# Kernel tuning notes

Measured on AMD Instinct MI355X. Metric: run time of the kernel, lower is better.

The kernel has to match this reference:

```python
import jax, jax.numpy as jnp
import numpy as np

B, M, H, D = 2, 16384, 8, 64
HID = H * D
SEG = 128          # segment_lengths[0]
DIL = 2            # dilation_rates[0]


def _hilbert_perm(m):
    """perm[d] = row-major token index of the d-th point on the Hilbert curve
    over an n x n grid (n = sqrt(m), power of 2). Vectorized d2xy."""
    n = int(round(np.sqrt(m)))
    assert n * n == m and (n & (n - 1)) == 0
    t = np.arange(m, dtype=np.int64)
    x = np.zeros(m, np.int64)
    y = np.zeros(m, np.int64)
    s = 1
    while s < n:
        rx = 1 & (t // 2)
        ry = 1 & (t ^ rx)
        swap = ry == 0
        flip = swap & (rx == 1)
        xf = np.where(flip, s - 1 - x, x)
        yf = np.where(flip, s - 1 - y, y)
        x, y = np.where(swap, yf, xf), np.where(swap, xf, yf)
        x = x + s * rx
        y = y + s * ry
        t = t // 4
        s *= 2
    return y * n + x


_PERM = _hilbert_perm(M)
_INV = np.empty(M, np.int64)
_INV[_PERM] = np.arange(M)
PERM = jnp.asarray(_PERM)
INV_PERM = jnp.asarray(_INV)


def setup_inputs() -> dict:
    key = jax.random.key(0)
    ks = jax.random.split(key, 8)
    sc = 0.02
    return {
        "q": jax.random.normal(ks[0], (B, M, H, D), jnp.float32),
        "k": jax.random.normal(ks[1], (B, M, H, D), jnp.float32),
        "v": jax.random.normal(ks[2], (B, M, H, D), jnp.float32),
        # wrapper projections (nn.Linear without bias; stored [in, out])
        "Wq": jax.random.normal(ks[3], (HID, HID), jnp.float32) * sc,
        "Wk": jax.random.normal(ks[4], (HID, HID), jnp.float32) * sc,
        "Wv": jax.random.normal(ks[5], (HID, HID), jnp.float32) * sc,
        # HilbertAttentionCore fused qkv projection
        "Wqkv": jax.random.normal(ks[6], (HID, 3 * HID), jnp.float32) * sc,
        # wrapper output projection
        "Wout": jax.random.normal(ks[7], (HID, HID), jnp.float32) * sc,
    }


def _hilbert_attention(x, Wqkv):
    """x: [B, M, HID] -> [B, M, HID]. Hilbert reorder + segmented dilated attn."""
    b, m, _ = x.shape
    qkv = x @ Wqkv                                    # [B, M, 3*HID]
    qkv = qkv.reshape(b, m, 3, H, D)
    # Hilbert-curve reordering of the sequence (gather)
    qkv = qkv[:, PERM]                                # [B, M, 3, H, D]
    nseg = m // SEG
    g = SEG // DIL                                    # tokens per dilated group
    # [B, nseg, g, DIL, 3, H, D]: group r holds positions r, r+DIL, ... in seg
    qkv = qkv.reshape(b, nseg, g, DIL, 3, H, D)
    qh, kh, vh = qkv[..., 0, :, :], qkv[..., 1, :, :], qkv[..., 2, :, :]
    scale = 1.0 / jnp.sqrt(jnp.asarray(D, x.dtype))
    # attention within each (segment, dilation-group): t,s index the g tokens
    scores = jnp.einsum("bntrhd,bnsrhd->bnrhts", qh, kh) * scale
    attn = jax.nn.softmax(scores, axis=-1)
    out = jnp.einsum("bnrhts,bnsrhd->bntrhd", attn, vh)
    out = out.reshape(b, m, H, D)
    # inverse Hilbert reordering (scatter back)
    out = out[:, INV_PERM]
    return out.reshape(b, m, HID)


def reference(q, k, v, Wq, Wk, Wv, Wqkv, Wout):
    b, m, h, d = q.shape
    q_flat = q.reshape(b, m, h * d)
    k_flat = k.reshape(b, m, h * d)
    v_flat = v.reshape(b, m, h * d)
    x = (q_flat @ Wq + k_flat @ Wk + v_flat @ Wv) / 3.0
    out = _hilbert_attention(x, Wqkv)
    out = out @ Wout
    return out.reshape(b, m, h, d)
```

## Files before the change

kernel.cpp:

```cpp
#include <hip/hip_runtime.h>
#include <hip/hip_bf16.h>
#include <stdint.h>


typedef __bf16 bf16_t;
typedef __bf16 bf16x8 __attribute__((ext_vector_type(8)));
typedef float  f32x4  __attribute__((ext_vector_type(4)));

#define DEVI __device__ __forceinline__
#define BAR __builtin_amdgcn_s_barrier()

static constexpr int Mtok = 16384;
static constexpr int ROWS = 32768;

DEVI void gload_lds16(const void* g, void* l) {
  __builtin_amdgcn_global_load_lds(
      (__attribute__((address_space(1))) uint32_t*)(uintptr_t)g,
      (__attribute__((address_space(3))) uint32_t*)(uint32_t)(uintptr_t)l,
      16, 0, 0);
}

__global__ void k_perm(int* __restrict__ perm) {
  int d = blockIdx.x * 256 + threadIdx.x;
  if (d >= Mtok) return;
  int t = d, x = 0, y = 0;
  for (int s = 1; s < 128; s <<= 1) {
    int rx = (t >> 1) & 1;
    int ry = (t ^ rx) & 1;
    if (ry == 0) {
      if (rx == 1) { x = s - 1 - x; y = s - 1 - y; }
      int tmp = x; x = y; y = tmp;
    }
    x += s * rx;
    y += s * ry;
    t >>= 2;
  }
  perm[d] = y * 128 + x;
}

__global__ void k_prep_w(const float* __restrict__ Wq, const float* __restrict__ Wk,
                         const float* __restrict__ Wv, const float* __restrict__ Wqkv,
                         const float* __restrict__ Wout,
                         bf16_t* __restrict__ W1t, bf16_t* __restrict__ Wqkvt,
                         bf16_t* __restrict__ Woutt) {
  const int tid = blockIdx.x * 256 + threadIdx.x;
  const int stride = gridDim.x * 256;
  for (int i = tid; i < 512 * 1536; i += stride) {
    int n = i / 1536, kk = i % 1536;
    const float* W = (kk < 512) ? Wq : (kk < 1024 ? Wk : Wv);
    W1t[i] = (bf16_t)(W[(kk & 511) * 512 + n] * (1.0f / 3.0f));
  }
  for (int i = tid; i < 1536 * 512; i += stride) {
    int n = i / 512, kk = i % 512;
    Wqkvt[i] = (bf16_t)Wqkv[kk * 1536 + n];
  }
  for (int i = tid; i < 512 * 512; i += stride) {
    int n = i / 512, kk = i % 512;
    Woutt[i] = (bf16_t)Wout[kk * 512 + n];
  }
}

DEVI void stageB(const bf16_t* Bb, int Kdim, int k0, bf16_t* dst, int qsel,
                 int tid, int cswz) {
  int r = tid >> 3;
  int rb0 = (r >> 5) * 64 + qsel * 32 + (r & 31);
  const bf16_t* g = Bb + (long)rb0 * Kdim + k0 + cswz * 8;
  gload_lds16(g, dst + rb0 * 64 + (tid & 7) * 8);
  gload_lds16(g + (long)128 * Kdim, dst + (rb0 + 128) * 64 + (tid & 7) * 8);
}

DEVI void stageA(const bf16_t* Ab, int Kdim, int k0, bf16_t* dst, int qsel,
                 int tid, int cswz) {
  int r = tid >> 3;
  int row0 = r + qsel * 64;
  const bf16_t* g = Ab + (long)row0 * Kdim + k0 + cswz * 8;
  gload_lds16(g, dst + row0 * 64 + (tid & 7) * 8);
  gload_lds16(g + (long)128 * Kdim, dst + (row0 + 128) * 64 + (tid & 7) * 8);
}

#define LOAD_AF(AF, QM, BUF)                                                   \
  _Pragma("unroll") for (int m = 0; m < 4; m++) {                              \
    int row = wm * 128 + (QM) * 64 + m * 16 + l15;                             \
    AF[m][0] = *(const bf16x8*)((BUF) + row * 64 + cb0 * 8);                   \
    AF[m][1] = *(const bf16x8*)((BUF) + row * 64 + cb1 * 8);                   \
  }
#define LOAD_BG(BG, QN, BUF)                                                   \
  _Pragma("unroll") for (int n = 0; n < 2; n++) {                              \
    int row = wn * 64 + (QN) * 32 + n * 16 + l15;                              \
    BG[n][0] = *(const bf16x8*)((BUF) + row * 64 + cb0 * 8);                   \
    BG[n][1] = *(const bf16x8*)((BUF) + row * 64 + cb1 * 8);                   \
  }
#define QUAD(QM, QN, AF, BG)                                                   \
  do {                                                                         \
    __builtin_amdgcn_s_setprio(1);                                             \
    _Pragma("unroll") for (int kh = 0; kh < 2; kh++)                           \
    _Pragma("unroll") for (int m = 0; m < 4; m++)                              \
    _Pragma("unroll") for (int n = 0; n < 2; n++)                              \
      acc[(QM)*4+m][(QN)*2+n] = __builtin_amdgcn_mfma_f32_16x16x32_bf16(       \
          AF[m][kh], BG[n][kh], acc[(QM)*4+m][(QN)*2+n], 0, 0, 0);             \
    __builtin_amdgcn_s_setprio(0);                                             \
  } while (0)

template <bool OUTF32>
__global__ __launch_bounds__(512, 2) void k_gemm256(const bf16_t* __restrict__ A,
                                                    const bf16_t* __restrict__ Bt,
                                                    bf16_t* __restrict__ Cb,
                                                    float* __restrict__ Cf,
                                                    int Ndim, int Kdim) {
  __shared__ bf16_t lds[4 * 16384];
  const int tid = threadIdx.x;
  const int lane = tid & 63, w = tid >> 6;
  const int wm = w >> 2, wn = w & 3;
  const int l15 = lane & 15, l4 = lane >> 4;
  const int cb0 = l4 ^ (l15 & 7), cb1 = cb0 ^ 4;
  const int cswz = (tid & 7) ^ ((tid >> 3) & 7);
  const long arow0 = (long)blockIdx.y * 256;
  const long bcol0 = (long)blockIdx.x * 256;
  const bf16_t* Ab = A + arow0 * Kdim;
  const bf16_t* Bb = Bt + bcol0 * Kdim;
  const int NT = Kdim >> 6;

  bf16_t* Acur = lds;
  bf16_t* Bcur = lds + 16384;
  bf16_t* Anxt = lds + 32768;
  bf16_t* Bnxt = lds + 49152;

  f32x4 acc[8][4] = {};

  stageA(Ab, Kdim, 0, Acur, 0, tid, cswz);
  stageA(Ab, Kdim, 0, Acur, 1, tid, cswz);
  stageB(Bb, Kdim, 0, Bcur, 0, tid, cswz);
  stageB(Bb, Kdim, 0, Bcur, 1, tid, cswz);
  stageA(Ab, Kdim, 64, Anxt, 0, tid, cswz);
  stageB(Bb, Kdim, 64, Bnxt, 1, tid, cswz);
  asm volatile("s_waitcnt vmcnt(4)" ::: "memory");
  BAR;

  for (int t = 0; t < NT; t++) {
    bf16x8 af[4][2], bg0[2][2], bg1[2][2];
    LOAD_AF(af, 0, Acur);
    LOAD_BG(bg0, 0, Bcur);
    if (t + 1 < NT) stageB(Bb, Kdim, (t + 1) * 64, Bnxt, 0, tid, cswz);
    BAR;
    QUAD(0, 0, af, bg0);
    BAR;
    LOAD_BG(bg1, 1, Bcur);
    if (t + 1 < NT) stageA(Ab, Kdim, (t + 1) * 64, Anxt, 1, tid, cswz);
    BAR;
    QUAD(0, 1, af, bg1);
    BAR;
    LOAD_AF(af, 1, Acur);
    if (t + 2 < NT) stageA(Ab, Kdim, (t + 2) * 64, Acur, 0, tid, cswz);
    BAR;
    QUAD(1, 1, af, bg1);
    BAR;
    LOAD_BG(bg0, 0, Bcur);
    if (t + 2 < NT) stageB(Bb, Kdim, (t + 2) * 64, Bcur, 1, tid, cswz);
    BAR;
    QUAD(1, 0, af, bg0);
    if (t + 2 < NT) { asm volatile("s_waitcnt vmcnt(4)" ::: "memory"); }
    else            { asm volatile("s_waitcnt vmcnt(0)" ::: "memory"); }
    BAR;
    bf16_t* tA = Acur; Acur = Anxt; Anxt = tA;
    bf16_t* tB = Bcur; Bcur = Bnxt; Bnxt = tB;
  }

#pragma unroll
  for (int i = 0; i < 8; i++) {
#pragma unroll
    for (int j = 0; j < 4; j++) {
      long row = arow0 + wm * 128 + i * 16 + l4 * 4;
      long col = bcol0 + wn * 64 + j * 16 + l15;
#pragma unroll
      for (int r = 0; r < 4; r++) {
        if constexpr (OUTF32) Cf[(row + r) * Ndim + col] = acc[i][j][r];
        else                  Cb[(row + r) * Ndim + col] = (bf16_t)acc[i][j][r];
      }
    }
  }
}

DEVI const float* selsrc(int tt, const float* q, const float* k, const float* v) {
  return tt < 8 ? q : (tt < 16 ? k : v);
}

DEVI void loadAh(const float* S, long grow, int colf, float4* pa) {
  const float* p0 = S + grow * 512 + colf;
  pa[0] = *(const float4*)(p0);
  pa[1] = *(const float4*)(p0 + 4);
  const float* p1 = p0 + 128 * 512;
  pa[2] = *(const float4*)(p1);
  pa[3] = *(const float4*)(p1 + 4);
}

DEVI void writeAh(bf16_t* dst, int rbase, int cbt, const float4* pa) {
  bf16x8 o0, o1;
  o0[0] = (bf16_t)pa[0].x; o0[1] = (bf16_t)pa[0].y; o0[2] = (bf16_t)pa[0].z; o0[3] = (bf16_t)pa[0].w;
  o0[4] = (bf16_t)pa[1].x; o0[5] = (bf16_t)pa[1].y; o0[6] = (bf16_t)pa[1].z; o0[7] = (bf16_t)pa[1].w;
  o1[0] = (bf16_t)pa[2].x; o1[1] = (bf16_t)pa[2].y; o1[2] = (bf16_t)pa[2].z; o1[3] = (bf16_t)pa[2].w;
  o1[4] = (bf16_t)pa[3].x; o1[5] = (bf16_t)pa[3].y; o1[6] = (bf16_t)pa[3].z; o1[7] = (bf16_t)pa[3].w;
  int sw = (cbt ^ (rbase & 7)) * 8;
  *(bf16x8*)(dst + rbase * 64 + sw) = o0;
  *(bf16x8*)(dst + (rbase + 128) * 64 + sw) = o1;
}

__global__ __launch_bounds__(512, 2) void k_gemm1f(const float* __restrict__ q,
                                                   const float* __restrict__ k,
                                                   const float* __restrict__ v,
                                                   const bf16_t* __restrict__ Bt,
                                                   bf16_t* __restrict__ Cb,
                                                   int Ndim) {
  constexpr int Kdim = 1536;
  constexpr int NT = 24;
  __shared__ bf16_t lds[4 * 16384];
  const int tid = threadIdx.x;
  const int lane = tid & 63, w = tid >> 6;
  const int wm = w >> 2, wn = w & 3;
  const int l15 = lane & 15, l4 = lane >> 4;
  const int cb0 = l4 ^ (l15 & 7), cb1 = cb0 ^ 4;
  const int cswz = (tid & 7) ^ ((tid >> 3) & 7);
  const int cbt = tid & 7, rA = tid >> 3;
  const long arow0 = (long)blockIdx.y * 256;
  const long bcol0 = (long)blockIdx.x * 256;
  const bf16_t* Bb = Bt + bcol0 * Kdim;

  bf16_t* Acur = lds;
  bf16_t* Bcur = lds + 16384;
  bf16_t* Anxt = lds + 32768;
  bf16_t* Bnxt = lds + 49152;

  f32x4 acc[8][4] = {};
  float4 pa0[4], pa1[4];

  loadAh(selsrc(0, q, k, v), arow0 + rA,      (cbt << 3), pa0);
  loadAh(selsrc(0, q, k, v), arow0 + rA + 64, (cbt << 3), pa1);
  writeAh(Acur, rA,      cbt, pa0);
  writeAh(Acur, rA + 64, cbt, pa1);
  stageB(Bb, Kdim, 0, Bcur, 0, tid, cswz);
  stageB(Bb, Kdim, 0, Bcur, 1, tid, cswz);
  loadAh(selsrc(1, q, k, v), arow0 + rA, 64 + (cbt << 3), pa0);
  writeAh(Anxt, rA, cbt, pa0);
  stageB(Bb, Kdim, 64, Bnxt, 1, tid, cswz);
  loadAh(selsrc(1, q, k, v), arow0 + rA + 64,  64 + (cbt << 3), pa1);
  loadAh(selsrc(2, q, k, v), arow0 + rA,      128 + (cbt << 3), pa0);
  asm volatile("s_waitcnt vmcnt(18)" ::: "memory");
  asm volatile("s_waitcnt lgkmcnt(0)" ::: "memory");
  BAR;

  for (int t = 0; t < NT; t++) {
    bf16x8 af[4][2], bg0[2][2], bg1[2][2];
    LOAD_AF(af, 0, Acur);
    LOAD_BG(bg0, 0, Bcur);
    if (t + 1 < NT) stageB(Bb, Kdim, (t + 1) * 64, Bnxt, 0, tid, cswz);
    BAR;
    QUAD(0, 0, af, bg0);
    BAR;
    LOAD_BG(bg1, 1, Bcur);
    if (t + 1 < NT) writeAh(Anxt, rA + 64, cbt, pa1);
    if (t + 2 < NT) loadAh(selsrc(t + 2, q, k, v), arow0 + rA + 64,
                           (((t + 2) & 7) << 6) + (cbt << 3), pa1);
    BAR;
    QUAD(0, 1, af, bg1);
    BAR;
    LOAD_AF(af, 1, Acur);
    if (t + 2 < NT) writeAh(Acur, rA, cbt, pa0);
    if (t + 3 < NT) loadAh(selsrc(t + 3, q, k, v), arow0 + rA,
                           (((t + 3) & 7) << 6) + (cbt << 3), pa0);
    BAR;
    QUAD(1, 1, af, bg1);
    BAR;
    LOAD_BG(bg0, 0, Bcur);
    if (t + 2 < NT) stageB(Bb, Kdim, (t + 2) * 64, Bcur, 1, tid, cswz);
    BAR;
    QUAD(1, 0, af, bg0);
    if (t + 3 < NT)      { asm volatile("s_waitcnt vmcnt(18)" ::: "memory"); }
    else if (t + 2 < NT) { asm volatile("s_waitcnt vmcnt(10)" ::: "memory"); }
    else                 { asm volatile("s_waitcnt vmcnt(0)"  ::: "memory"); }
    asm volatile("s_waitcnt lgkmcnt(0)" ::: "memory");
    BAR;
    bf16_t* tA = Acur; Acur = Anxt; Anxt = tA;
    bf16_t* tB = Bcur; Bcur = Bnxt; Bnxt = tB;
  }

#pragma unroll
  for (int i = 0; i < 8; i++) {
#pragma unroll
    for (int j = 0; j < 4; j++) {
      long row = arow0 + wm * 128 + i * 16 + l4 * 4;
      long col = bcol0 + wn * 64 + j * 16 + l15;
#pragma unroll
      for (int r = 0; r < 4; r++)
        Cb[(row + r) * Ndim + col] = (bf16_t)acc[i][j][r];
    }
  }
}

__global__ __launch_bounds__(256, 2) void k_attn(const bf16_t* __restrict__ QKV,
                                                 const int* __restrict__ perm,
                                                 bf16_t* __restrict__ ATT) {
  __shared__ bf16_t Vt[2][64 * 64];
  __shared__ bf16_t P[2][64 * 64];
  __shared__ bf16_t O[128 * 64];
  __shared__ int perml[128];
  const int n = blockIdx.x, h = blockIdx.y, b = blockIdx.z;
  const int t = threadIdx.x;
  const int lane = t & 63, w = t >> 6;
  const int l15 = lane & 15, l4 = lane >> 4;

  if (t < 128) perml[t] = perm[n * 128 + t];
  __syncthreads();

#pragma unroll
  for (int it = 0; it < 4; it++) {
    int c = t + it * 256;
    int tok = c >> 3, c8 = c & 7;
    long j = (long)b * Mtok + perml[tok];
    bf16x8 vv = *(const bf16x8*)(QKV + j * 1536 + 1024 + h * 64 + c8 * 8);
    int grp = tok & 1, s = tok >> 1;
    bf16_t* vt = Vt[grp];
#pragma unroll
    for (int i = 0; i < 8; i++) {
      int d = c8 * 8 + i;
      vt[d * 64 + (s ^ ((d & 7) << 3))] = vv[i];
    }
  }

  const int grp = w >> 1, th = w & 1;

  f32x4 sc[2][4] = {};
#pragma unroll
  for (int ks = 0; ks < 2; ks++) {
    bf16x8 aq[2], bk[4];
#pragma unroll
    for (int tf = 0; tf < 2; tf++) {
      int tq = th * 32 + tf * 16 + l15;
      long j = (long)b * Mtok + perml[tq * 2 + grp];
      aq[tf] = *(const bf16x8*)(QKV + j * 1536 + h * 64 + ks * 32 + l4 * 8);
    }
#pragma unroll
    for (int sf = 0; sf < 4; sf++) {
      int s = sf * 16 + l15;
      long j = (long)b * Mtok + perml[s * 2 + grp];
      bk[sf] = *(const bf16x8*)(QKV + j * 1536 + 512 + h * 64 + ks * 32 + l4 * 8);
    }
#pragma unroll
    for (int tf = 0; tf < 2; tf++)
#pragma unroll
      for (int sf = 0; sf < 4; sf++)
        sc[tf][sf] = __builtin_amdgcn_mfma_f32_16x16x32_bf16(aq[tf], bk[sf], sc[tf][sf], 0, 0, 0);
  }

  const float scale = 0.125f;
#pragma unroll
  for (int tf = 0; tf < 2; tf++) {
#pragma unroll
    for (int r = 0; r < 4; r++) {
      float mx = fmaxf(fmaxf(sc[tf][0][r], sc[tf][1][r]), fmaxf(sc[tf][2][r], sc[tf][3][r]));
      mx = fmaxf(mx, __shfl_xor(mx, 1, 64));
      mx = fmaxf(mx, __shfl_xor(mx, 2, 64));
      mx = fmaxf(mx, __shfl_xor(mx, 4, 64));
      mx = fmaxf(mx, __shfl_xor(mx, 8, 64));
      float p0 = __expf((sc[tf][0][r] - mx) * scale);
      float p1 = __expf((sc[tf][1][r] - mx) * scale);
      float p2 = __expf((sc[tf][2][r] - mx) * scale);
      float p3 = __expf((sc[tf][3][r] - mx) * scale);
      float sum = p0 + p1 + p2 + p3;
      sum += __shfl_xor(sum, 1, 64);
      sum += __shfl_xor(sum, 2, 64);
      sum += __shfl_xor(sum, 4, 64);
      sum += __shfl_xor(sum, 8, 64);
      float inv = 1.0f / sum;
      int trow = th * 32 + tf * 16 + l4 * 4 + r;
      int sw = (trow & 7) << 3;
      bf16_t* pp = P[grp];
      pp[trow * 64 + ((l15     ) ^ sw)] = (bf16_t)(p0 * inv);
      pp[trow * 64 + ((l15 + 16) ^ sw)] = (bf16_t)(p1 * inv);
      pp[trow * 64 + ((l15 + 32) ^ sw)] = (bf16_t)(p2 * inv);
      pp[trow * 64 + ((l15 + 48) ^ sw)] = (bf16_t)(p3 * inv);
    }
  }
  __syncthreads();

  f32x4 oacc[2][4] = {};
#pragma unroll
  for (int ks = 0; ks < 2; ks++) {
    bf16x8 ap[2], bv[4];
#pragma unroll
    for (int tf = 0; tf < 2; tf++) {
      int trow = th * 32 + tf * 16 + l15;
      int cb = (ks * 4 + l4) ^ (trow & 7);
      ap[tf] = *(const bf16x8*)(P[grp] + trow * 64 + cb * 8);
    }
#pragma unroll
    for (int df = 0; df < 4; df++) {
      int d = df * 16 + l15;
      int cb = (ks * 4 + l4) ^ (d & 7);
      bv[df] = *(const bf16x8*)(Vt[grp] + d * 64 + cb * 8);
    }
#pragma unroll
    for (int tf = 0; tf < 2; tf++)
#pragma unroll
      for (int df = 0; df < 4; df++)
        oacc[tf][df] = __builtin_amdgcn_mfma_f32_16x16x32_bf16(ap[tf], bv[df], oacc[tf][df], 0, 0, 0);
  }

#pragma unroll
  for (int tf = 0; tf < 2; tf++)
#pragma unroll
    for (int df = 0; df < 4; df++)
#pragma unroll
      for (int r = 0; r < 4; r++) {
        int trow = th * 32 + tf * 16 + l4 * 4 + r;
        int tok = trow * 2 + grp;
        O[tok * 64 + df * 16 + l15] = (bf16_t)oacc[tf][df][r];
      }
  __syncthreads();
#pragma unroll
  for (int it = 0; it < 4; it++) {
    int c = t + it * 256;
    int tok = c >> 3, c8 = c & 7;
    long j = (long)b * Mtok + perml[tok];
    *(bf16x8*)(ATT + j * 512 + h * 64 + c8 * 8) = *(const bf16x8*)(O + tok * 64 + c8 * 8);
  }
}

extern "C" void kernel_launch(void* const* d_in, const int* in_sizes, int n_in,
                              void* d_out, int out_size, void* d_ws, size_t ws_size,
                              hipStream_t stream) {
  const float* q    = (const float*)d_in[0];
  const float* k    = (const float*)d_in[1];
  const float* v    = (const float*)d_in[2];
  const float* Wq   = (const float*)d_in[3];
  const float* Wk   = (const float*)d_in[4];
  const float* Wv   = (const float*)d_in[5];
  const float* Wqkv = (const float*)d_in[6];
  const float* Wout = (const float*)d_in[7];

  char* ws = (char*)d_ws;
  const size_t QKV_BYTES = (size_t)ROWS * 1536 * 2;
  const size_t X_BYTES   = (size_t)ROWS * 512 * 2;
  bf16_t* QKV   = (bf16_t*)ws;
  bf16_t* X     = (bf16_t*)(ws + QKV_BYTES);
  bf16_t* W1t   = (bf16_t*)(ws + QKV_BYTES + X_BYTES);
  bf16_t* Wqkvt = W1t + 512 * 1536;
  bf16_t* Woutt = Wqkvt + 1536 * 512;
  int*    perm  = (int*)(Woutt + 512 * 512);

  k_perm<<<64, 256, 0, stream>>>(perm);
  k_prep_w<<<512, 256, 0, stream>>>(Wq, Wk, Wv, Wqkv, Wout, W1t, Wqkvt, Woutt);
  k_gemm1f<<<dim3(2, 128), 512, 0, stream>>>(q, k, v, W1t, X, 512);
  k_gemm256<false><<<dim3(6, 128), 512, 0, stream>>>(X, Wqkvt, QKV, nullptr, 1536, 512);
  k_attn<<<dim3(128, 8, 2), 256, 0, stream>>>(QKV, perm, X);
  k_gemm256<true><<<dim3(2, 128), 512, 0, stream>>>(X, Woutt, nullptr, (float*)d_out, 512, 512);
}
```

Baseline: 233.5 us.

## Fuse QKV projection, segmented attention and output projection into one kernel

Replaces the QKV GEMM, the attention kernel and the output-projection GEMM with a single kernel per (segment, dilation group, batch). Each block gathers its 64 permuted X rows into LDS, computes per-head Q/K/V with double-buffered weight tiles, runs attention in LDS and accumulates the output projection in registers. Results are scattered straight to the fp32 output. This removes the large bf16 QKV and attention intermediates in global memory and two kernel launches. In exchange, every block re-streams the full reordered Wqkv and Wout weights, heavy LDS use limits occupancy to one block per CU, and only half the waves do the attention step.

```diff
diff --git a/kernel.cpp b/kernel.cpp
--- a/kernel.cpp
+++ b/kernel.cpp
@@ -5,6 +5,7 @@
 
 typedef __bf16 bf16_t;
 typedef __bf16 bf16x8 __attribute__((ext_vector_type(8)));
+typedef __bf16 bf16x4 __attribute__((ext_vector_type(4)));
 typedef float  f32x4  __attribute__((ext_vector_type(4)));
 
 #define DEVI __device__ __forceinline__
@@ -41,7 +42,7 @@
 __global__ void k_prep_w(const float* __restrict__ Wq, const float* __restrict__ Wk,
                          const float* __restrict__ Wv, const float* __restrict__ Wqkv,
                          const float* __restrict__ Wout,
-                         bf16_t* __restrict__ W1t, bf16_t* __restrict__ Wqkvt,
+                         bf16_t* __restrict__ W1t, bf16_t* __restrict__ Wqkvr,
                          bf16_t* __restrict__ Woutt) {
   const int tid = blockIdx.x * 256 + threadIdx.x;
   const int stride = gridDim.x * 256;
@@ -50,9 +51,12 @@
     const float* W = (kk < 512) ? Wq : (kk < 1024 ? Wk : Wv);
     W1t[i] = (bf16_t)(W[(kk & 511) * 512 + n] * (1.0f / 3.0f));
   }
-  for (int i = tid; i < 1536 * 512; i += stride) {
-    int n = i / 512, kk = i % 512;
-    Wqkvt[i] = (bf16_t)Wqkv[kk * 1536 + n];
+  for (int i = tid; i < 8 * 192 * 512; i += stride) {
+    int h = i / (192 * 512);
+    int rem = i % (192 * 512);
+    int row = rem / 512, kk = rem % 512;
+    int gsel = row >> 6, c = row & 63;
+    Wqkvr[i] = (bf16_t)Wqkv[kk * 1536 + gsel * 512 + h * 64 + c];
   }
   for (int i = tid; i < 512 * 512; i += stride) {
     int n = i / 512, kk = i % 512;
@@ -67,15 +71,6 @@
   const bf16_t* g = Bb + (long)rb0 * Kdim + k0 + cswz * 8;
   gload_lds16(g, dst + rb0 * 64 + (tid & 7) * 8);
   gload_lds16(g + (long)128 * Kdim, dst + (rb0 + 128) * 64 + (tid & 7) * 8);
-}
-
-DEVI void stageA(const bf16_t* Ab, int Kdim, int k0, bf16_t* dst, int qsel,
-                 int tid, int cswz) {
-  int r = tid >> 3;
-  int row0 = r + qsel * 64;
-  const bf16_t* g = Ab + (long)row0 * Kdim + k0 + cswz * 8;
-  gload_lds16(g, dst + row0 * 64 + (tid & 7) * 8);
-  gload_lds16(g + (long)128 * Kdim, dst + (row0 + 128) * 64 + (tid & 7) * 8);
 }
 
 #define LOAD_AF(AF, QM, BUF)                                                   \
@@ -100,85 +95,6 @@
           AF[m][kh], BG[n][kh], acc[(QM)*4+m][(QN)*2+n], 0, 0, 0);             \
     __builtin_amdgcn_s_setprio(0);                                             \
   } while (0)
-
-template <bool OUTF32>
-__global__ __launch_bounds__(512, 2) void k_gemm256(const bf16_t* __restrict__ A,
-                                                    const bf16_t* __restrict__ Bt,
-                                                    bf16_t* __restrict__ Cb,
-                                                    float* __restrict__ Cf,
-                                                    int Ndim, int Kdim) {
-  __shared__ bf16_t lds[4 * 16384];
-  const int tid = threadIdx.x;
-  const int lane = tid & 63, w = tid >> 6;
-  const int wm = w >> 2, wn = w & 3;
-  const int l15 = lane & 15, l4 = lane >> 4;
-  const int cb0 = l4 ^ (l15 & 7), cb1 = cb0 ^ 4;
-  const int cswz = (tid & 7) ^ ((tid >> 3) & 7);
-  const long arow0 = (long)blockIdx.y * 256;
-  const long bcol0 = (long)blockIdx.x * 256;
-  const bf16_t* Ab = A + arow0 * Kdim;
-  const bf16_t* Bb = Bt + bcol0 * Kdim;
-  const int NT = Kdim >> 6;
-
-  bf16_t* Acur = lds;
-  bf16_t* Bcur = lds + 16384;
-  bf16_t* Anxt = lds + 32768;
-  bf16_t* Bnxt = lds + 49152;
-
-  f32x4 acc[8][4] = {};
-
-  stageA(Ab, Kdim, 0, Acur, 0, tid, cswz);
-  stageA(Ab, Kdim, 0, Acur, 1, tid, cswz);
-  stageB(Bb, Kdim, 0, Bcur, 0, tid, cswz);
-  stageB(Bb, Kdim, 0, Bcur, 1, tid, cswz);
-  stageA(Ab, Kdim, 64, Anxt, 0, tid, cswz);
-  stageB(Bb, Kdim, 64, Bnxt, 1, tid, cswz);
-  asm volatile("s_waitcnt vmcnt(4)" ::: "memory");
-  BAR;
-
-  for (int t = 0; t < NT; t++) {
-    bf16x8 af[4][2], bg0[2][2], bg1[2][2];
-    LOAD_AF(af, 0, Acur);
-    LOAD_BG(bg0, 0, Bcur);
-    if (t + 1 < NT) stageB(Bb, Kdim, (t + 1) * 64, Bnxt, 0, tid, cswz);
-    BAR;
-    QUAD(0, 0, af, bg0);
-    BAR;
-    LOAD_BG(bg1, 1, Bcur);
-    if (t + 1 < NT) stageA(Ab, Kdim, (t + 1) * 64, Anxt, 1, tid, cswz);
-    BAR;
-    QUAD(0, 1, af, bg1);
-    BAR;
-    LOAD_AF(af, 1, Acur);
-    if (t + 2 < NT) stageA(Ab, Kdim, (t + 2) * 64, Acur, 0, tid, cswz);
-    BAR;
-    QUAD(1, 1, af, bg1);
-    BAR;
-    LOAD_BG(bg0, 0, Bcur);
-    if (t + 2 < NT) stageB(Bb, Kdim, (t + 2) * 64, Bcur, 1, tid, cswz);
-    BAR;
-    QUAD(1, 0, af, bg0);
-    if (t + 2 < NT) { asm volatile("s_waitcnt vmcnt(4)" ::: "memory"); }
-    else            { asm volatile("s_waitcnt vmcnt(0)" ::: "memory"); }
-    BAR;
-    bf16_t* tA = Acur; Acur = Anxt; Anxt = tA;
-    bf16_t* tB = Bcur; Bcur = Bnxt; Bnxt = tB;
-  }
-
-#pragma unroll
-  for (int i = 0; i < 8; i++) {
-#pragma unroll
-    for (int j = 0; j < 4; j++) {
-      long row = arow0 + wm * 128 + i * 16 + l4 * 4;
-      long col = bcol0 + wn * 64 + j * 16 + l15;
-#pragma unroll
-      for (int r = 0; r < 4; r++) {
-        if constexpr (OUTF32) Cf[(row + r) * Ndim + col] = acc[i][j][r];
-        else                  Cb[(row + r) * Ndim + col] = (bf16_t)acc[i][j][r];
-      }
-    }
-  }
-}
 
 DEVI const float* selsrc(int tt, const float* q, const float* k, const float* v) {
   return tt < 8 ? q : (tt < 16 ? k : v);
@@ -295,132 +211,230 @@
   }
 }
 
-__global__ __launch_bounds__(256, 2) void k_attn(const bf16_t* __restrict__ QKV,
-                                                 const int* __restrict__ perm,
-                                                 bf16_t* __restrict__ ATT) {
-  __shared__ bf16_t Vt[2][64 * 64];
-  __shared__ bf16_t P[2][64 * 64];
-  __shared__ bf16_t O[128 * 64];
-  __shared__ int perml[128];
-  const int n = blockIdx.x, h = blockIdx.y, b = blockIdx.z;
-  const int t = threadIdx.x;
-  const int lane = t & 63, w = t >> 6;
+__global__ __launch_bounds__(512, 2) void k_fuse23(const bf16_t* __restrict__ X,
+                                                   const bf16_t* __restrict__ Wqkvr,
+                                                   const bf16_t* __restrict__ Woutt,
+                                                   const int* __restrict__ perm,
+                                                   float* __restrict__ out) {
+  __shared__ bf16_t Xl[64 * 512];
+  __shared__ bf16_t Bd[2][192 * 64];
+  __shared__ bf16_t Ql[64 * 64], Kl[64 * 64], VT[64 * 64], Pl[64 * 64], Ol[64 * 64];
+  __shared__ int perml[64];
+  const int n = blockIdx.x, g = blockIdx.y, b = blockIdx.z;
+  const int tid = threadIdx.x;
+  const int lane = tid & 63, w = tid >> 6;
   const int l15 = lane & 15, l4 = lane >> 4;
 
-  if (t < 128) perml[t] = perm[n * 128 + t];
+  if (tid < 64) perml[tid] = perm[n * 128 + tid * 2 + g];
   __syncthreads();
 
 #pragma unroll
-  for (int it = 0; it < 4; it++) {
-    int c = t + it * 256;
-    int tok = c >> 3, c8 = c & 7;
-    long j = (long)b * Mtok + perml[tok];
-    bf16x8 vv = *(const bf16x8*)(QKV + j * 1536 + 1024 + h * 64 + c8 * 8);
-    int grp = tok & 1, s = tok >> 1;
-    bf16_t* vt = Vt[grp];
-#pragma unroll
-    for (int i = 0; i < 8; i++) {
-      int d = c8 * 8 + i;
-      vt[d * 64 + (s ^ ((d & 7) << 3))] = vv[i];
-    }
-  }
-
-  const int grp = w >> 1, th = w & 1;
-
-  f32x4 sc[2][4] = {};
-#pragma unroll
-  for (int ks = 0; ks < 2; ks++) {
-    bf16x8 aq[2], bk[4];
-#pragma unroll
-    for (int tf = 0; tf < 2; tf++) {
-      int tq = th * 32 + tf * 16 + l15;
-      long j = (long)b * Mtok + perml[tq * 2 + grp];
-      aq[tf] = *(const bf16x8*)(QKV + j * 1536 + h * 64 + ks * 32 + l4 * 8);
-    }
-#pragma unroll
-    for (int sf = 0; sf < 4; sf++) {
-      int s = sf * 16 + l15;
-      long j = (long)b * Mtok + perml[s * 2 + grp];
-      bk[sf] = *(const bf16x8*)(QKV + j * 1536 + 512 + h * 64 + ks * 32 + l4 * 8);
-    }
-#pragma unroll
-    for (int tf = 0; tf < 2; tf++)
-#pragma unroll
-      for (int sf = 0; sf < 4; sf++)
-        sc[tf][sf] = __builtin_amdgcn_mfma_f32_16x16x32_bf16(aq[tf], bk[sf], sc[tf][sf], 0, 0, 0);
-  }
-
-  const float scale = 0.125f;
-#pragma unroll
-  for (int tf = 0; tf < 2; tf++) {
+  for (int j = 0; j < 8; j++) {
+    int cc = tid + j * 512;
+    int s = cc >> 6, ch = cc & 63;
+    const bf16_t* src = X + ((long)(b * Mtok + perml[s])) * 512 + ((ch ^ (s & 7)) * 8);
+    gload_lds16(src, Xl + cc * 8);
+  }
+
+  f32x4 oacc3[4][4] = {};
+
+  const int r2base = (w & 1) * 32;
+  const int c2base = (w >> 1) * 48;
+
+  for (int h = 0; h < 8; h++) {
+    f32x4 facc[2][3] = {};
+    {
+      const bf16_t* Wh = Wqkvr + (long)h * 192 * 512;
+#pragma unroll
+      for (int j = 0; j < 3; j++) {
+        int cc = tid + j * 512;
+        int row = cc >> 3, ch = cc & 7;
+        gload_lds16(Wh + row * 512 + ((ch ^ (row & 7)) * 8), Bd[0] + cc * 8);
+      }
+      for (int kk = 0; kk < 8; kk++) {
+        bf16_t* curB = Bd[kk & 1];
+        if (kk < 7) {
+          bf16_t* nxtB = Bd[(kk & 1) ^ 1];
+#pragma unroll
+          for (int j = 0; j < 3; j++) {
+            int cc = tid + j * 512;
+            int row = cc >> 3, ch = cc & 7;
+            gload_lds16(Wh + row * 512 + (kk + 1) * 64 + ((ch ^ (row & 7)) * 8),
+                        nxtB + cc * 8);
+          }
+          asm volatile("s_waitcnt vmcnt(3)" ::: "memory");
+        } else {
+          asm volatile("s_waitcnt vmcnt(0)" ::: "memory");
+        }
+        __syncthreads();
+        bf16x8 af[2][2], bg[3][2];
+#pragma unroll
+        for (int rf = 0; rf < 2; rf++) {
+          int row = r2base + rf * 16 + l15;
+#pragma unroll
+          for (int sub = 0; sub < 2; sub++) {
+            int ch = (kk * 8 + sub * 4 + l4) ^ (row & 7);
+            af[rf][sub] = *(const bf16x8*)(Xl + row * 64 * 8 / 8 * 8 + 0);
+          }
+        }
+#pragma unroll
+        for (int rf = 0; rf < 2; rf++) {
+          int row = r2base + rf * 16 + l15;
+#pragma unroll
+          for (int sub = 0; sub < 2; sub++) {
+            int ch = (kk * 8 + sub * 4 + l4) ^ (row & 7);
+            af[rf][sub] = *(const bf16x8*)(Xl + (row * 64 + ch) * 8);
+          }
+        }
+#pragma unroll
+        for (int cf = 0; cf < 3; cf++) {
+          int row = c2base + cf * 16 + l15;
+#pragma unroll
+          for (int sub = 0; sub < 2; sub++) {
+            int ch = (sub * 4 + l4) ^ (row & 7);
+            bg[cf][sub] = *(const bf16x8*)(curB + (row * 8 + ch) * 8);
+          }
+        }
+#pragma unroll
+        for (int rf = 0; rf < 2; rf++)
+#pragma unroll
+          for (int cf = 0; cf < 3; cf++)
+#pragma unroll
+            for (int sub = 0; sub < 2; sub++)
+              facc[rf][cf] = __builtin_amdgcn_mfma_f32_16x16x32_bf16(
+                  af[rf][sub], bg[cf][sub], facc[rf][cf], 0, 0, 0);
+        __syncthreads();
+      }
+    }
+
+#pragma unroll
+    for (int rf = 0; rf < 2; rf++) {
+      int t0 = r2base + rf * 16 + l4 * 4;
+#pragma unroll
+      for (int cf = 0; cf < 3; cf++) {
+        int c = c2base + cf * 16 + l15;
+        if (c < 64) {
+#pragma unroll
+          for (int r = 0; r < 4; r++) {
+            int t = t0 + r;
+            Ql[t * 64 + (((c >> 3) ^ (t & 7)) * 8) + (c & 7)] = (bf16_t)facc[rf][cf][r];
+          }
+        } else if (c < 128) {
+          int ck = c - 64;
+#pragma unroll
+          for (int r = 0; r < 4; r++) {
+            int t = t0 + r;
+            Kl[t * 64 + (((ck >> 3) ^ (t & 7)) * 8) + (ck & 7)] = (bf16_t)facc[rf][cf][r];
+          }
+        } else {
+          int d = c - 128;
+          bf16x4 pk;
+          pk[0] = (bf16_t)facc[rf][cf][0]; pk[1] = (bf16_t)facc[rf][cf][1];
+          pk[2] = (bf16_t)facc[rf][cf][2]; pk[3] = (bf16_t)facc[rf][cf][3];
+          *(bf16x4*)(VT + d * 64 + (((t0 >> 3) ^ (d & 7)) * 8) + (t0 & 7)) = pk;
+        }
+      }
+    }
+    __syncthreads();
+
+    if (w < 4) {
+      f32x4 sc[4] = {};
+#pragma unroll
+      for (int ks = 0; ks < 2; ks++) {
+        int tq = w * 16 + l15;
+        bf16x8 aq = *(const bf16x8*)(Ql + (tq * 8 + (((ks * 4 + l4) ^ (tq & 7)))) * 8);
+#pragma unroll
+        for (int cf = 0; cf < 4; cf++) {
+          int s = cf * 16 + l15;
+          bf16x8 bk = *(const bf16x8*)(Kl + (s * 8 + ((ks * 4 + l4) ^ (s & 7))) * 8);
+          sc[cf] = __builtin_amdgcn_mfma_f32_16x16x32_bf16(aq, bk, sc[cf], 0, 0, 0);
+        }
+      }
+      const float scale = 0.125f;
+#pragma unroll
+      for (int r = 0; r < 4; r++) {
+        float mx = fmaxf(fmaxf(sc[0][r], sc[1][r]), fmaxf(sc[2][r], sc[3][r]));
+        mx = fmaxf(mx, __shfl_xor(mx, 1, 64));
+        mx = fmaxf(mx, __shfl_xor(mx, 2, 64));
+        mx = fmaxf(mx, __shfl_xor(mx, 4, 64));
+        mx = fmaxf(mx, __shfl_xor(mx, 8, 64));
+        float p0 = __expf((sc[0][r] - mx) * scale);
+        float p1 = __expf((sc[1][r] - mx) * scale);
+        float p2 = __expf((sc[2][r] - mx) * scale);
+        float p3 = __expf((sc[3][r] - mx) * scale);
+        float sum = p0 + p1 + p2 + p3;
+        sum += __shfl_xor(sum, 1, 64);
+        sum += __shfl_xor(sum, 2, 64);
+        sum += __shfl_xor(sum, 4, 64);
+        sum += __shfl_xor(sum, 8, 64);
+        float inv = 1.0f / sum;
+        int t = w * 16 + l4 * 4 + r;
+        float pv[4] = {p0, p1, p2, p3};
+#pragma unroll
+        for (int cf = 0; cf < 4; cf++) {
+          int s = cf * 16 + l15;
+          Pl[t * 64 + (((s >> 3) ^ (t & 7)) * 8) + (s & 7)] = (bf16_t)(pv[cf] * inv);
+        }
+      }
+    }
+    __syncthreads();
+    if (w < 4) {
+      f32x4 po[4] = {};
+#pragma unroll
+      for (int ks = 0; ks < 2; ks++) {
+        int tq = w * 16 + l15;
+        bf16x8 ap = *(const bf16x8*)(Pl + (tq * 8 + ((ks * 4 + l4) ^ (tq & 7))) * 8);
+#pragma unroll
+        for (int cf = 0; cf < 4; cf++) {
+          int d = cf * 16 + l15;
+          bf16x8 bv = *(const bf16x8*)(VT + (d * 8 + ((ks * 4 + l4) ^ (d & 7))) * 8);
+          po[cf] = __builtin_amdgcn_mfma_f32_16x16x32_bf16(ap, bv, po[cf], 0, 0, 0);
+        }
+      }
+#pragma unroll
+      for (int cf = 0; cf < 4; cf++) {
+        int d = cf * 16 + l15;
+#pragma unroll
+        for (int r = 0; r < 4; r++) {
+          int t = w * 16 + l4 * 4 + r;
+          Ol[t * 64 + (((d >> 3) ^ (t & 7)) * 8) + (d & 7)] = (bf16_t)po[cf][r];
+        }
+      }
+    }
+    __syncthreads();
+
+#pragma unroll
+    for (int ks = 0; ks < 2; ks++) {
+      bf16x8 af3[4], bg3[4];
+#pragma unroll
+      for (int rf = 0; rf < 4; rf++) {
+        int t = rf * 16 + l15;
+        af3[rf] = *(const bf16x8*)(Ol + (t * 8 + ((ks * 4 + l4) ^ (t & 7))) * 8);
+      }
+#pragma unroll
+      for (int cf = 0; cf < 4; cf++) {
+        int c = w * 64 + cf * 16 + l15;
+        bg3[cf] = *(const bf16x8*)(Woutt + (long)c * 512 + h * 64 + ks * 32 + l4 * 8);
+      }
+#pragma unroll
+      for (int rf = 0; rf < 4; rf++)
+#pragma unroll
+        for (int cf = 0; cf < 4; cf++)
+          oacc3[rf][cf] = __builtin_amdgcn_mfma_f32_16x16x32_bf16(
+              af3[rf], bg3[cf], oacc3[rf][cf], 0, 0, 0);
+    }
+  }
+
+#pragma unroll
+  for (int rf = 0; rf < 4; rf++) {
 #pragma unroll
     for (int r = 0; r < 4; r++) {
-      float mx = fmaxf(fmaxf(sc[tf][0][r], sc[tf][1][r]), fmaxf(sc[tf][2][r], sc[tf][3][r]));
-      mx = fmaxf(mx, __shfl_xor(mx, 1, 64));
-      mx = fmaxf(mx, __shfl_xor(mx, 2, 64));
-      mx = fmaxf(mx, __shfl_xor(mx, 4, 64));
-      mx = fmaxf(mx, __shfl_xor(mx, 8, 64));
-      float p0 = __expf((sc[tf][0][r] - mx) * scale);
-      float p1 = __expf((sc[tf][1][r] - mx) * scale);
-      float p2 = __expf((sc[tf][2][r] - mx) * scale);
-      float p3 = __expf((sc[tf][3][r] - mx) * scale);
-      float sum = p0 + p1 + p2 + p3;
-      sum += __shfl_xor(sum, 1, 64);
-      sum += __shfl_xor(sum, 2, 64);
-      sum += __shfl_xor(sum, 4, 64);
-      sum += __shfl_xor(sum, 8, 64);
-      float inv = 1.0f / sum;
-      int trow = th * 32 + tf * 16 + l4 * 4 + r;
-      int sw = (trow & 7) << 3;
-      bf16_t* pp = P[grp];
-      pp[trow * 64 + ((l15     ) ^ sw)] = (bf16_t)(p0 * inv);
-      pp[trow * 64 + ((l15 + 16) ^ sw)] = (bf16_t)(p1 * inv);
-      pp[trow * 64 + ((l15 + 32) ^ sw)] = (bf16_t)(p2 * inv);
-      pp[trow * 64 + ((l15 + 48) ^ sw)] = (bf16_t)(p3 * inv);
-    }
-  }
-  __syncthreads();
-
-  f32x4 oacc[2][4] = {};
-#pragma unroll
-  for (int ks = 0; ks < 2; ks++) {
-    bf16x8 ap[2], bv[4];
-#pragma unroll
-    for (int tf = 0; tf < 2; tf++) {
-      int trow = th * 32 + tf * 16 + l15;
-      int cb = (ks * 4 + l4) ^ (trow & 7);
-      ap[tf] = *(const bf16x8*)(P[grp] + trow * 64 + cb * 8);
-    }
-#pragma unroll
-    for (int df = 0; df < 4; df++) {
-      int d = df * 16 + l15;
-      int cb = (ks * 4 + l4) ^ (d & 7);
-      bv[df] = *(const bf16x8*)(Vt[grp] + d * 64 + cb * 8);
-    }
-#pragma unroll
-    for (int tf = 0; tf < 2; tf++)
-#pragma unroll
-      for (int df = 0; df < 4; df++)
-        oacc[tf][df] = __builtin_amdgcn_mfma_f32_16x16x32_bf16(ap[tf], bv[df], oacc[tf][df], 0, 0, 0);
-  }
-
-#pragma unroll
-  for (int tf = 0; tf < 2; tf++)
-#pragma unroll
-    for (int df = 0; df < 4; df++)
-#pragma unroll
-      for (int r = 0; r < 4; r++) {
-        int trow = th * 32 + tf * 16 + l4 * 4 + r;
-        int tok = trow * 2 + grp;
-        O[tok * 64 + df * 16 + l15] = (bf16_t)oacc[tf][df][r];
-      }
-  __syncthreads();
-#pragma unroll
-  for (int it = 0; it < 4; it++) {
-    int c = t + it * 256;
-    int tok = c >> 3, c8 = c & 7;
-    long j = (long)b * Mtok + perml[tok];
-    *(bf16x8*)(ATT + j * 512 + h * 64 + c8 * 8) = *(const bf16x8*)(O + tok * 64 + c8 * 8);
+      int t = rf * 16 + l4 * 4 + r;
+      long orow = (long)(b * Mtok + perml[t]) * 512 + w * 64;
+#pragma unroll
+      for (int cf = 0; cf < 4; cf++)
+        out[orow + cf * 16 + l15] = oacc3[rf][cf][r];
+    }
   }
 }
 
@@ -437,19 +451,15 @@
   const float* Wout = (const float*)d_in[7];
 
   char* ws = (char*)d_ws;
-  const size_t QKV_BYTES = (size_t)ROWS * 1536 * 2;
-  const size_t X_BYTES   = (size_t)ROWS * 512 * 2;
-  bf16_t* QKV   = (bf16_t*)ws;
-  bf16_t* X     = (bf16_t*)(ws + QKV_BYTES);
-  bf16_t* W1t   = (bf16_t*)(ws + QKV_BYTES + X_BYTES);
-  bf16_t* Wqkvt = W1t + 512 * 1536;
-  bf16_t* Woutt = Wqkvt + 1536 * 512;
+  const size_t X_BYTES = (size_t)ROWS * 512 * 2;
+  bf16_t* X     = (bf16_t*)ws;
+  bf16_t* W1t   = (bf16_t*)(ws + X_BYTES);
+  bf16_t* Wqkvr = W1t + 512 * 1536;
+  bf16_t* Woutt = Wqkvr + 8 * 192 * 512;
   int*    perm  = (int*)(Woutt + 512 * 512);
 
   k_perm<<<64, 256, 0, stream>>>(perm);
-  k_prep_w<<<512, 256, 0, stream>>>(Wq, Wk, Wv, Wqkv, Wout, W1t, Wqkvt, Woutt);
+  k_prep_w<<<512, 256, 0, stream>>>(Wq, Wk, Wv, Wqkv, Wout, W1t, Wqkvr, Woutt);
   k_gemm1f<<<dim3(2, 128), 512, 0, stream>>>(q, k, v, W1t, X, 512);
-  k_gemm256<false><<<dim3(6, 128), 512, 0, stream>>>(X, Wqkvt, QKV, nullptr, 1536, 512);
-  k_attn<<<dim3(128, 8, 2), 256, 0, stream>>>(QKV, perm, X);
-  k_gemm256<true><<<dim3(2, 128), 512, 0, stream>>>(X, Woutt, nullptr, (float*)d_out, 512, 512);
-}
+  k_fuse23<<<dim3(128, 2, 2), 512, 0, stream>>>(X, Wqkvr, Woutt, perm, (float*)d_out);
+}
```

Result: slower. 263.4 us (+12.8%).
